# Kernel tuning notes

Hardware: AMD Instinct MI355X
Metric: run time of the kernel (lower is better)

## Reference

```python
import jax, jax.numpy as jnp
import numpy as np

N_U, N_I, E = 100000, 100000, 600000
F_U, F_I, H, OUT = 96, 160, 128, 64
EPS = 1e-5


def _params(key):
    ks = jax.random.split(key, 20)
    n = lambda i, s: (jax.random.normal(ks[i], s, jnp.float32) * 0.05)
    p = {
        # lazy per-type input projections
        'Wp_u': n(0, (F_U, H)), 'bp_u': jnp.zeros((H,), jnp.float32),
        'Wp_i': n(1, (F_I, H)), 'bp_i': jnp.zeros((H,), jnp.float32),
        # layer 0 SAGE (in=H, out=H): lin_l (neighbors, bias), lin_r (root, no bias)
        'Wl0_ui': n(2, (H, H)), 'bl0_ui': jnp.zeros((H,), jnp.float32), 'Wr0_ui': n(3, (H, H)),
        'Wl0_iu': n(4, (H, H)), 'bl0_iu': jnp.zeros((H,), jnp.float32), 'Wr0_iu': n(5, (H, H)),
        'g0_u': jnp.ones((H,), jnp.float32), 'b0_u': jnp.zeros((H,), jnp.float32),
        'g0_i': jnp.ones((H,), jnp.float32), 'b0_i': jnp.zeros((H,), jnp.float32),
        # layer 1 SAGE (in=H, out=OUT)
        'Wl1_ui': n(6, (H, OUT)), 'bl1_ui': jnp.zeros((OUT,), jnp.float32), 'Wr1_ui': n(7, (H, OUT)),
        'Wl1_iu': n(8, (H, OUT)), 'bl1_iu': jnp.zeros((OUT,), jnp.float32), 'Wr1_iu': n(9, (H, OUT)),
        'g1_u': jnp.ones((OUT,), jnp.float32), 'b1_u': jnp.zeros((OUT,), jnp.float32),
        'g1_i': jnp.ones((OUT,), jnp.float32), 'b1_i': jnp.zeros((OUT,), jnp.float32),
    }
    return p


def setup_inputs() -> dict:
    key = jax.random.key(0)
    k0, k1, k2, k3, kp = jax.random.split(key, 5)
    inp = {
        'x_user': jax.random.normal(k0, (N_U, F_U), jnp.float32),
        'x_item': jax.random.normal(k1, (N_I, F_I), jnp.float32),
        'edge_ui': jax.random.randint(k2, (2, E), 0, N_U),  # row0: src user idx, row1: dst item idx
        'edge_iu': jax.random.randint(k3, (2, E), 0, N_I),  # row0: src item idx, row1: dst user idx
    }
    inp.update(_params(kp))
    return inp


def _seg_mean(x_src, src, dst, n_dst):
    # gather source features [E, C], scatter-mean into destinations [n_dst, C]
    msg = x_src[src]
    s = jax.ops.segment_sum(msg, dst, num_segments=n_dst)
    cnt = jax.ops.segment_sum(jnp.ones((dst.shape[0], 1), x_src.dtype), dst, num_segments=n_dst)
    return s / jnp.maximum(cnt, 1.0)


def _sage(x_src, x_dst, edge, Wl, bl, Wr, n_dst):
    agg = _seg_mean(x_src, edge[0], edge[1], n_dst)
    return agg @ Wl + bl + x_dst @ Wr


def _ln(h, g, b):
    m = jnp.mean(h, axis=-1, keepdims=True)
    v = jnp.mean(jnp.square(h - m), axis=-1, keepdims=True)
    return (h - m) * jax.lax.rsqrt(v + EPS) * g + b


def reference(x_user, x_item, edge_ui, edge_iu,
              Wp_u, bp_u, Wp_i, bp_i,
              Wl0_ui, bl0_ui, Wr0_ui, Wl0_iu, bl0_iu, Wr0_iu,
              g0_u, b0_u, g0_i, b0_i,
              Wl1_ui, bl1_ui, Wr1_ui, Wl1_iu, bl1_iu, Wr1_iu,
              g1_u, b1_u, g1_i, b1_i):
    # per-type input projection + ReLU
    h_u = jax.nn.relu(x_user @ Wp_u + bp_u)
    h_i = jax.nn.relu(x_item @ Wp_i + bp_i)
    # layer 0: HeteroConv(sum) of SAGEConv per edge type, then per-type LN + ReLU (dropout = eval identity)
    h_i1 = _sage(h_u, h_i, edge_ui, Wl0_ui, bl0_ui, Wr0_ui, N_I)
    h_u1 = _sage(h_i, h_u, edge_iu, Wl0_iu, bl0_iu, Wr0_iu, N_U)
    h_u1 = jax.nn.relu(_ln(h_u1, g0_u, b0_u))
    h_i1 = jax.nn.relu(_ln(h_i1, g0_i, b0_i))
    # layer 1 (final): SAGE -> LN, no ReLU/dropout
    h_i2 = _sage(h_u1, h_i1, edge_ui, Wl1_ui, bl1_ui, Wr1_ui, N_I)
    h_u2 = _sage(h_i1, h_u1, edge_iu, Wl1_iu, bl1_iu, Wr1_iu, N_U)
    h_u2 = _ln(h_u2, g1_u, b1_u)
    h_i2 = _ln(h_i2, g1_i, b1_i)
    return h_u2, h_i2
```

## Files before the change

### kernel.cpp

```cpp
#include <hip/hip_runtime.h>

typedef __attribute__((ext_vector_type(8))) __bf16 bf16x8;
typedef __attribute__((ext_vector_type(4))) float floatx4;
typedef __attribute__((ext_vector_type(8))) unsigned short ushort8v;
typedef __attribute__((ext_vector_type(4))) unsigned short ushort4v;

namespace {
constexpr int kNU = 100000, kNI = 100000, kE = 600000;
constexpr int kFU = 96, kFI = 160, kH = 128, kOUT = 64;
constexpr float kEPS = 1e-5f;
constexpr int kM = 32;
constexpr int kNCHUNK = 98;
constexpr int kNBLK = kNU / kM;
constexpr int kEB = (kE + 255) / 256;
}

__device__ __forceinline__ unsigned short f2b(float f) {
  unsigned u = __builtin_bit_cast(unsigned, f);
  u += 0x7FFFu + ((u >> 16) & 1u);
  return (unsigned short)(u >> 16);
}
__device__ __forceinline__ float b2f(unsigned short h) {
  return __builtin_bit_cast(float, (unsigned)h << 16);
}
__device__ __forceinline__ void split3(float v, unsigned short& h,
                                       unsigned short& m, unsigned short& l) {
  h = f2b(v);
  const float r1 = v - b2f(h);
  m = f2b(r1);
  const float r2 = r1 - b2f(m);
  l = f2b(r2);
}
__device__ __forceinline__ void split2(float v, unsigned short& h,
                                       unsigned short& m) {
  h = f2b(v);
  m = f2b(v - b2f(h));
}
__device__ __forceinline__ bf16x8 ldb8(const unsigned short* p) {
  return __builtin_bit_cast(bf16x8, *(const ushort8v*)p);
}
__device__ __forceinline__ floatx4 mfma16(bf16x8 a, bf16x8 b, floatx4 c) {
  return __builtin_amdgcn_mfma_f32_16x16x32_bf16(a, b, c, 0, 0, 0);
}
__device__ __forceinline__ unsigned short* ab_ptr(unsigned short* base,
                                                  int plane, int r, int bo) {
  return (unsigned short*)((char*)base + plane * 8192 + r * 256 +
                           (bo ^ ((r & 7) << 4)));
}

struct WcvtArgs {
  const float* src[10];
  unsigned short* dh[10];
  unsigned short* dm[10];
  unsigned short* dl[10];
  int K[10], N[10];
};
__global__ __launch_bounds__(256) void wcvt(WcvtArgs a) {
  const int m = blockIdx.y;
  const int K = a.K[m], N = a.N[m];
  const int idx = blockIdx.x * 256 + threadIdx.x;
  if (idx < K * N) {
    const int n = idx / K, k = idx - n * K;
    unsigned short h, mm, l;
    split3(a.src[m][(size_t)k * N + n], h, mm, l);
    a.dh[m][idx] = h;
    a.dm[m][idx] = mm;
    a.dl[m][idx] = l;
  }
}

__global__ void zero_int(int* __restrict__ p, int n) {
  int i = blockIdx.x * blockDim.x + threadIdx.x;
  const int st = gridDim.x * blockDim.x;
  for (; i < n; i += st) p[i] = 0;
}

__global__ __launch_bounds__(1024) void scanA(const int* __restrict__ cnt_u,
                                              const int* __restrict__ cnt_i,
                                              int* ptr_u, int* ptr_i, int* tot) {
  __shared__ int sh[1024];
  const int dir = blockIdx.y;
  const int* cnt = dir ? cnt_i : cnt_u;
  int* ptr = dir ? ptr_i : ptr_u;
  const int t = threadIdx.x;
  const int i = blockIdx.x * 1024 + t;
  const int v = (i < kNU) ? cnt[i] : 0;
  sh[t] = v;
  __syncthreads();
  for (int o = 1; o < 1024; o <<= 1) {
    const int y = (t >= o) ? sh[t - o] : 0;
    __syncthreads();
    sh[t] += y;
    __syncthreads();
  }
  if (i < kNU) ptr[i] = sh[t] - v;
  if (t == 1023) tot[dir * 128 + blockIdx.x] = sh[1023];
}

__global__ __launch_bounds__(128) void scanB(int* tot) {
  __shared__ int sh[128];
  int* tp = tot + blockIdx.x * 128;
  const int t = threadIdx.x;
  const int v = (t < kNCHUNK) ? tp[t] : 0;
  sh[t] = v;
  __syncthreads();
  for (int o = 1; o < 128; o <<= 1) {
    const int y = (t >= o) ? sh[t - o] : 0;
    __syncthreads();
    sh[t] += y;
    __syncthreads();
  }
  if (t < kNCHUNK) tp[t] = sh[t] - v;
}

__global__ __launch_bounds__(1024) void scanC(int* ptr_u, int* ptr_i,
                                              const int* __restrict__ tot,
                                              int* cur_u, int* cur_i) {
  const int dir = blockIdx.y;
  int* ptr = dir ? ptr_i : ptr_u;
  int* cur = dir ? cur_i : cur_u;
  const int i = blockIdx.x * 1024 + threadIdx.x;
  if (i < kNU) {
    const int v = ptr[i] + tot[dir * 128 + blockIdx.x];
    ptr[i] = v;
    cur[i] = v;
  }
}

template <int F>
__device__ __forceinline__ void proj_body(
    const float* __restrict__ x, const unsigned short* __restrict__ Wh,
    const unsigned short* __restrict__ Wm, const unsigned short* __restrict__ Wl,
    const float* __restrict__ bias, float* __restrict__ out, int blk,
    unsigned short* sh) {
  constexpr int AS = F + 8, KC = F / 32;
  unsigned short* Ah = sh;
  unsigned short* Am = sh + kM * AS;
  unsigned short* Al = sh + 2 * kM * AS;
  const int tid = threadIdx.x;
  const size_t row0 = (size_t)blk * kM;
  for (int c = tid; c < kM * (F / 4); c += 256) {
    const int r = c / (F / 4), j = c % (F / 4);
    const float4 v = *(const float4*)&x[(row0 + r) * F + j * 4];
    const float* vv = &v.x;
    ushort4v h4, m4, l4;
#pragma unroll
    for (int u = 0; u < 4; ++u) {
      unsigned short th, tm, tl;
      split3(vv[u], th, tm, tl);
      h4[u] = th; m4[u] = tm; l4[u] = tl;
    }
    *(ushort4v*)&Ah[r * AS + j * 4] = h4;
    *(ushort4v*)&Am[r * AS + j * 4] = m4;
    *(ushort4v*)&Al[r * AS + j * 4] = l4;
  }
  const int lane = tid & 63, w = tid >> 6, q = lane >> 4, ln = lane & 15;
  floatx4 acc[2][2] = {}, accL[2][2] = {};
  __syncthreads();
#pragma unroll
  for (int kc = 0; kc < KC; ++kc) {
    bf16x8 bh[2], bm[2], bl_[2];
#pragma unroll
    for (int t = 0; t < 2; ++t) {
      const int off = (w * 32 + t * 16 + ln) * F + kc * 32 + q * 8;
      bh[t] = ldb8(&Wh[off]);
      bm[t] = ldb8(&Wm[off]);
      bl_[t] = ldb8(&Wl[off]);
    }
#pragma unroll
    for (int mt = 0; mt < 2; ++mt) {
      const int ro = mt * 16 + ln, co = kc * 32 + q * 8;
      const bf16x8 ah = ldb8(&Ah[ro * AS + co]);
      const bf16x8 am = ldb8(&Am[ro * AS + co]);
      const bf16x8 al = ldb8(&Al[ro * AS + co]);
#pragma unroll
      for (int t = 0; t < 2; ++t) {
        acc[mt][t] = mfma16(ah, bh[t], acc[mt][t]);
        floatx4 cl = accL[mt][t];
        cl = mfma16(ah, bm[t], cl);
        cl = mfma16(am, bh[t], cl);
        cl = mfma16(ah, bl_[t], cl);
        cl = mfma16(al, bh[t], cl);
        cl = mfma16(am, bm[t], cl);
        accL[mt][t] = cl;
      }
    }
  }
#pragma unroll
  for (int t = 0; t < 2; ++t) {
    const int col = w * 32 + t * 16 + ln;
    const float bv = bias[col];
#pragma unroll
    for (int mt = 0; mt < 2; ++mt)
#pragma unroll
      for (int r = 0; r < 4; ++r)
        out[(row0 + mt * 16 + q * 4 + r) * kH + col] =
            fmaxf((acc[mt][t][r] + accL[mt][t][r]) + bv, 0.f);
  }
}

__global__ __launch_bounds__(256) void hist_proj(
    const int* __restrict__ eui, const int* __restrict__ eiu, int* cnt_i,
    int* cnt_u, const float* __restrict__ x,
    const unsigned short* __restrict__ Wh, const unsigned short* __restrict__ Wm,
    const unsigned short* __restrict__ Wl, const float* __restrict__ bias,
    float* __restrict__ out) {
  __shared__ __align__(16) unsigned short sh[3 * kM * (kFU + 8)];
  if (blockIdx.x < kEB) {
    const int e = blockIdx.x * 256 + threadIdx.x;
    if (e < kE) {
      atomicAdd(&cnt_i[eui[kE + e]], 1);
      atomicAdd(&cnt_u[eiu[kE + e]], 1);
    }
  } else {
    proj_body<kFU>(x, Wh, Wm, Wl, bias, out, blockIdx.x - kEB, sh);
  }
}

__global__ __launch_bounds__(256) void fill_proj(
    const int* __restrict__ eui, const int* __restrict__ eiu, int* cur_i,
    int* cur_u, int* __restrict__ col_ui, int* __restrict__ col_iu,
    const float* __restrict__ x, const unsigned short* __restrict__ Wh,
    const unsigned short* __restrict__ Wm, const unsigned short* __restrict__ Wl,
    const float* __restrict__ bias, float* __restrict__ out) {
  __shared__ __align__(16) unsigned short sh[3 * kM * (kFI + 8)];
  if (blockIdx.x < kEB) {
    const int e = blockIdx.x * 256 + threadIdx.x;
    if (e < kE) {
      const int p = atomicAdd(&cur_i[eui[kE + e]], 1);
      col_ui[p] = eui[e];
      const int p2 = atomicAdd(&cur_u[eiu[kE + e]], 1);
      col_iu[p2] = eiu[e];
    }
  } else {
    proj_body<kFI>(x, Wh, Wm, Wl, bias, out, blockIdx.x - kEB, sh);
  }
}

struct AggArgs {
  const float* src[2];
  const int* ptr[2];
  const int* cur[2];
  const int* col[2];
  float* out[2];
};
template <int W>
__global__ __launch_bounds__(256) void agg2(AggArgs a) {
  const int dir = blockIdx.y;
  const int w = threadIdx.x >> 6, lane = threadIdx.x & 63;
  const int row = blockIdx.x * 4 + w;
  const float* __restrict__ feat = a.src[dir];
  const int* __restrict__ col = a.col[dir];
  const int beg = a.ptr[dir][row], end = a.cur[dir][row];
  const float inv = 1.0f / fmaxf((float)(end - beg), 1.0f);
  if (W == 128) {
    float s0 = 0.f, s1 = 0.f;
    int e = beg;
    for (; e + 4 <= end; e += 4) {
      const size_t c0 = col[e], c1 = col[e + 1], c2 = col[e + 2],
                   c3 = col[e + 3];
      const float2 v0 = *(const float2*)&feat[c0 * 128 + lane * 2];
      const float2 v1 = *(const float2*)&feat[c1 * 128 + lane * 2];
      const float2 v2 = *(const float2*)&feat[c2 * 128 + lane * 2];
      const float2 v3 = *(const float2*)&feat[c3 * 128 + lane * 2];
      s0 += v0.x; s1 += v0.y;
      s0 += v1.x; s1 += v1.y;
      s0 += v2.x; s1 += v2.y;
      s0 += v3.x; s1 += v3.y;
    }
    for (; e < end; ++e) {
      const float2 v = *(const float2*)&feat[(size_t)col[e] * 128 + lane * 2];
      s0 += v.x; s1 += v.y;
    }
    float2 o;
    o.x = s0 * inv;
    o.y = s1 * inv;
    *(float2*)&a.out[dir][(size_t)row * 128 + lane * 2] = o;
  } else {
    float s = 0.f;
    int e = beg;
    for (; e + 4 <= end; e += 4) {
      const size_t c0 = col[e], c1 = col[e + 1], c2 = col[e + 2],
                   c3 = col[e + 3];
      const float v0 = feat[c0 * 64 + lane];
      const float v1 = feat[c1 * 64 + lane];
      const float v2 = feat[c2 * 64 + lane];
      const float v3 = feat[c3 * 64 + lane];
      s += v0; s += v1; s += v2; s += v3;
    }
    for (; e < end; ++e) s += feat[(size_t)col[e] * 64 + lane];
    a.out[dir][(size_t)row * 64 + lane] = s * inv;
  }
}

struct FsArgs {
  const float* agg[2];
  const float* root[2];
  const unsigned short *WLh[2], *WLm[2], *WLl[2];
  const unsigned short *WRh[2], *WRm[2], *WRl[2];
  const float *bl[2], *g[2], *b[2];
  float* out[2];
};
__global__ __launch_bounds__(256) void sage0(FsArgs a) {
  constexpr int NOUT = 128;
  __shared__ __align__(16) unsigned short Ab[4 * kM * kH];
  float* Cs = (float*)Ab;
  const int tid = threadIdx.x;
  const int dir = blockIdx.y;
  const size_t row0 = (size_t)blockIdx.x * kM;
  const float* __restrict__ agg = a.agg[dir];
  const float* __restrict__ root = a.root[dir];

  for (int c = tid; c < 2048; c += 256) {
    const int mat = c >> 10, cc = c & 1023, r = cc >> 5, j = cc & 31;
    const float4 v = *(const float4*)((mat ? root : agg) + (row0 + r) * kH + j * 4);
    const float* vv = &v.x;
    ushort4v h4, m4;
#pragma unroll
    for (int u = 0; u < 4; ++u) {
      unsigned short th, tm;
      split2(vv[u], th, tm);
      h4[u] = th; m4[u] = tm;
    }
    *(ushort4v*)ab_ptr(Ab, mat * 2 + 0, r, j * 8) = h4;
    *(ushort4v*)ab_ptr(Ab, mat * 2 + 1, r, j * 8) = m4;
  }

  const int lane = tid & 63, w = tid >> 6, q = lane >> 4, ln = lane & 15;
  floatx4 acc[2][2] = {}, accL[2][2] = {};
  const unsigned short* __restrict__ WLh = a.WLh[dir];
  const unsigned short* __restrict__ WLm = a.WLm[dir];
  const unsigned short* __restrict__ WLl = a.WLl[dir];
  const unsigned short* __restrict__ WRh = a.WRh[dir];
  const unsigned short* __restrict__ WRm = a.WRm[dir];
  const unsigned short* __restrict__ WRl = a.WRl[dir];
  __syncthreads();
#pragma unroll
  for (int kc = 0; kc < 4; ++kc) {
    bf16x8 BL[3][2], BR[3][2];
#pragma unroll
    for (int t = 0; t < 2; ++t) {
      const int off = (w * 32 + t * 16 + ln) * kH + kc * 32 + q * 8;
      BL[0][t] = ldb8(&WLh[off]);
      BL[1][t] = ldb8(&WLm[off]);
      BL[2][t] = ldb8(&WLl[off]);
      BR[0][t] = ldb8(&WRh[off]);
      BR[1][t] = ldb8(&WRm[off]);
      BR[2][t] = ldb8(&WRl[off]);
    }
#pragma unroll
    for (int mt = 0; mt < 2; ++mt) {
      const int ro = mt * 16 + ln, cob = kc * 64 + q * 16;
      const bf16x8 a1h = ldb8(ab_ptr(Ab, 0, ro, cob));
      const bf16x8 a1m = ldb8(ab_ptr(Ab, 1, ro, cob));
      const bf16x8 a2h = ldb8(ab_ptr(Ab, 2, ro, cob));
      const bf16x8 a2m = ldb8(ab_ptr(Ab, 3, ro, cob));
#pragma unroll
      for (int t = 0; t < 2; ++t) {
        floatx4 c = acc[mt][t];
        c = mfma16(a1h, BL[0][t], c);
        c = mfma16(a2h, BR[0][t], c);
        acc[mt][t] = c;
        floatx4 cl = accL[mt][t];
        cl = mfma16(a1h, BL[1][t], cl);
        cl = mfma16(a1m, BL[0][t], cl);
        cl = mfma16(a1h, BL[2][t], cl);
        cl = mfma16(a1m, BL[1][t], cl);
        cl = mfma16(a2h, BR[1][t], cl);
        cl = mfma16(a2m, BR[0][t], cl);
        cl = mfma16(a2h, BR[2][t], cl);
        cl = mfma16(a2m, BR[1][t], cl);
        accL[mt][t] = cl;
      }
    }
  }
  __syncthreads();
  const float* __restrict__ blv = a.bl[dir];
#pragma unroll
  for (int t = 0; t < 2; ++t) {
    const int colx = (w * 2 + t) * 16 + ln;
    const float bv = blv[colx];
#pragma unroll
    for (int mt = 0; mt < 2; ++mt)
#pragma unroll
      for (int r = 0; r < 4; ++r)
        Cs[(mt * 16 + q * 4 + r) * (NOUT + 1) + colx] =
            (acc[mt][t][r] + accL[mt][t][r]) + bv;
  }
  __syncthreads();
  const int r = tid >> 3, sub = tid & 7;
  const float* __restrict__ gg = a.g[dir];
  const float* __restrict__ bb = a.b[dir];
  float vals[16], s = 0.f;
#pragma unroll
  for (int j = 0; j < 16; ++j) {
    const float v = Cs[r * (NOUT + 1) + sub * 16 + j];
    vals[j] = v;
    s += v;
  }
#pragma unroll
  for (int o = 1; o < 8; o <<= 1) s += __shfl_xor(s, o, 64);
  const float mean = s * (1.0f / NOUT);
  float s2 = 0.f;
#pragma unroll
  for (int j = 0; j < 16; ++j) {
    const float d = vals[j] - mean;
    s2 += d * d;
  }
#pragma unroll
  for (int o = 1; o < 8; o <<= 1) s2 += __shfl_xor(s2, o, 64);
  const float rstd = rsqrtf(s2 * (1.0f / NOUT) + kEPS);
  float* op = a.out[dir] + (row0 + r) * NOUT + sub * 16;
#pragma unroll
  for (int j = 0; j < 16; j += 4) {
    float4 o4;
    float* oo = &o4.x;
#pragma unroll
    for (int jj = 0; jj < 4; ++jj)
      oo[jj] = fmaxf((vals[j + jj] - mean) * rstd * gg[sub * 16 + j + jj] +
                         bb[sub * 16 + j + jj],
                     0.f);
    *(float4*)&op[j] = o4;
  }
}

struct ZArgs {
  const float* src[2];
  const unsigned short *Bh[2], *Bm[2], *Bl[2];
  float* out[2];
};
__global__ __launch_bounds__(256) void zproj(ZArgs a) {
  __shared__ __align__(16) unsigned short Ab[2 * kM * kH];
  const int tid = threadIdx.x, dir = blockIdx.y;
  const size_t row0 = (size_t)blockIdx.x * kM;
  const float* __restrict__ src = a.src[dir];
  for (int c = tid; c < 1024; c += 256) {
    const int r = c >> 5, j = c & 31;
    const float4 v = *(const float4*)&src[(row0 + r) * kH + j * 4];
    const float* vv = &v.x;
    ushort4v h4, m4;
#pragma unroll
    for (int u = 0; u < 4; ++u) {
      unsigned short th, tm;
      split2(vv[u], th, tm);
      h4[u] = th; m4[u] = tm;
    }
    *(ushort4v*)ab_ptr(Ab, 0, r, j * 8) = h4;
    *(ushort4v*)ab_ptr(Ab, 1, r, j * 8) = m4;
  }
  const int lane = tid & 63, w = tid >> 6, q = lane >> 4, ln = lane & 15;
  const unsigned short* __restrict__ Bh = a.Bh[dir];
  const unsigned short* __restrict__ Bm = a.Bm[dir];
  const unsigned short* __restrict__ Bl = a.Bl[dir];
  floatx4 acc[2] = {}, accL[2] = {};
  __syncthreads();
#pragma unroll
  for (int kc = 0; kc < 4; ++kc) {
    const int off = (w * 16 + ln) * kH + kc * 32 + q * 8;
    const bf16x8 bh = ldb8(&Bh[off]);
    const bf16x8 bm = ldb8(&Bm[off]);
    const bf16x8 bl_ = ldb8(&Bl[off]);
#pragma unroll
    for (int mt = 0; mt < 2; ++mt) {
      const int ro = mt * 16 + ln, cob = kc * 64 + q * 16;
      const bf16x8 ah = ldb8(ab_ptr(Ab, 0, ro, cob));
      const bf16x8 am = ldb8(ab_ptr(Ab, 1, ro, cob));
      acc[mt] = mfma16(ah, bh, acc[mt]);
      floatx4 cl = accL[mt];
      cl = mfma16(ah, bm, cl);
      cl = mfma16(am, bh, cl);
      cl = mfma16(ah, bl_, cl);
      cl = mfma16(am, bm, cl);
      accL[mt] = cl;
    }
  }
  float* __restrict__ out = a.out[dir];
  const int col = w * 16 + ln;
#pragma unroll
  for (int mt = 0; mt < 2; ++mt)
#pragma unroll
    for (int r = 0; r < 4; ++r)
      out[(row0 + mt * 16 + q * 4 + r) * kOUT + col] =
          acc[mt][r] + accL[mt][r];
}

struct S1Args {
  const float* root[2];
  const float* aggz[2];
  const unsigned short *Bh[2], *Bm[2], *Bl[2];
  const float *bl[2], *g[2], *b[2];
  float* out[2];
};
__global__ __launch_bounds__(256) void sage1(S1Args a) {
  constexpr int NOUT = kOUT;
  __shared__ __align__(16) unsigned short Ab[2 * kM * kH];
  float* Cs = (float*)Ab;
  const int tid = threadIdx.x, dir = blockIdx.y;
  const size_t row0 = (size_t)blockIdx.x * kM;
  const float* __restrict__ root = a.root[dir];
  for (int c = tid; c < 1024; c += 256) {
    const int r = c >> 5, j = c & 31;
    const float4 v = *(const float4*)&root[(row0 + r) * kH + j * 4];
    const float* vv = &v.x;
    ushort4v h4, m4;
#pragma unroll
    for (int u = 0; u < 4; ++u) {
      unsigned short th, tm;
      split2(vv[u], th, tm);
      h4[u] = th; m4[u] = tm;
    }
    *(ushort4v*)ab_ptr(Ab, 0, r, j * 8) = h4;
    *(ushort4v*)ab_ptr(Ab, 1, r, j * 8) = m4;
  }
  const int lane = tid & 63, w = tid >> 6, q = lane >> 4, ln = lane & 15;
  const unsigned short* __restrict__ Bh = a.Bh[dir];
  const unsigned short* __restrict__ Bm = a.Bm[dir];
  const unsigned short* __restrict__ Bl = a.Bl[dir];
  floatx4 acc[2] = {}, accL[2] = {};
  __syncthreads();
#pragma unroll
  for (int kc = 0; kc < 4; ++kc) {
    const int off = (w * 16 + ln) * kH + kc * 32 + q * 8;
    const bf16x8 bh = ldb8(&Bh[off]);
    const bf16x8 bm = ldb8(&Bm[off]);
    const bf16x8 bl_ = ldb8(&Bl[off]);
#pragma unroll
    for (int mt = 0; mt < 2; ++mt) {
      const int ro = mt * 16 + ln, cob = kc * 64 + q * 16;
      const bf16x8 ah = ldb8(ab_ptr(Ab, 0, ro, cob));
      const bf16x8 am = ldb8(ab_ptr(Ab, 1, ro, cob));
      acc[mt] = mfma16(ah, bh, acc[mt]);
      floatx4 cl = accL[mt];
      cl = mfma16(ah, bm, cl);
      cl = mfma16(am, bh, cl);
      cl = mfma16(ah, bl_, cl);
      cl = mfma16(am, bm, cl);
      accL[mt] = cl;
    }
  }
  __syncthreads();
  const float* __restrict__ blv = a.bl[dir];
  {
    const int col = w * 16 + ln;
    const float bv = blv[col];
#pragma unroll
    for (int mt = 0; mt < 2; ++mt)
#pragma unroll
      for (int r = 0; r < 4; ++r)
        Cs[(mt * 16 + q * 4 + r) * (NOUT + 1) + col] =
            (acc[mt][r] + accL[mt][r]) + bv;
  }
  __syncthreads();
  const int r = tid >> 3, sub = tid & 7;
  const float* __restrict__ az = a.aggz[dir];
  const float* __restrict__ gg = a.g[dir];
  const float* __restrict__ bb = a.b[dir];
  float vals[8], s = 0.f;
#pragma unroll
  for (int j = 0; j < 8; ++j) {
    const float v = Cs[r * (NOUT + 1) + sub * 8 + j] +
                    az[(row0 + r) * NOUT + sub * 8 + j];
    vals[j] = v;
    s += v;
  }
#pragma unroll
  for (int o = 1; o < 8; o <<= 1) s += __shfl_xor(s, o, 64);
  const float mean = s * (1.0f / NOUT);
  float s2 = 0.f;
#pragma unroll
  for (int j = 0; j < 8; ++j) {
    const float d = vals[j] - mean;
    s2 += d * d;
  }
#pragma unroll
  for (int o = 1; o < 8; o <<= 1) s2 += __shfl_xor(s2, o, 64);
  const float rstd = rsqrtf(s2 * (1.0f / NOUT) + kEPS);
  float* op = a.out[dir] + (row0 + r) * NOUT + sub * 8;
#pragma unroll
  for (int j = 0; j < 8; j += 4) {
    float4 o4;
    float* oo = &o4.x;
#pragma unroll
    for (int jj = 0; jj < 4; ++jj)
      oo[jj] = (vals[j + jj] - mean) * rstd * gg[sub * 8 + j + jj] +
               bb[sub * 8 + j + jj];
    *(float4*)&op[j] = o4;
  }
}

extern "C" void kernel_launch(void* const* d_in, const int* in_sizes, int n_in,
                              void* d_out, int out_size, void* d_ws, size_t ws_size,
                              hipStream_t stream) {
  (void)in_sizes; (void)n_in; (void)out_size; (void)ws_size;
  const float* x_u    = (const float*)d_in[0];
  const float* x_i    = (const float*)d_in[1];
  const int*   e_ui   = (const int*)d_in[2];
  const int*   e_iu   = (const int*)d_in[3];
  const float* Wp_u   = (const float*)d_in[4];
  const float* bp_u   = (const float*)d_in[5];
  const float* Wp_i   = (const float*)d_in[6];
  const float* bp_i   = (const float*)d_in[7];
  const float* Wl0_ui = (const float*)d_in[8];
  const float* bl0_ui = (const float*)d_in[9];
  const float* Wr0_ui = (const float*)d_in[10];
  const float* Wl0_iu = (const float*)d_in[11];
  const float* bl0_iu = (const float*)d_in[12];
  const float* Wr0_iu = (const float*)d_in[13];
  const float* g0_u   = (const float*)d_in[14];
  const float* b0_u   = (const float*)d_in[15];
  const float* g0_i   = (const float*)d_in[16];
  const float* b0_i   = (const float*)d_in[17];
  const float* Wl1_ui = (const float*)d_in[18];
  const float* bl1_ui = (const float*)d_in[19];
  const float* Wr1_ui = (const float*)d_in[20];
  const float* Wl1_iu = (const float*)d_in[21];
  const float* bl1_iu = (const float*)d_in[22];
  const float* Wr1_iu = (const float*)d_in[23];
  const float* g1_u   = (const float*)d_in[24];
  const float* b1_u   = (const float*)d_in[25];
  const float* g1_i   = (const float*)d_in[26];
  const float* b1_i   = (const float*)d_in[27];

  float* pf = (float*)d_ws;
  const size_t NH = (size_t)kNU * kH;
  float* hu0 = pf;
  float* hi0 = pf + NH;
  float* b2  = pf + 2 * NH;
  float* b3  = pf + 3 * NH;
  float* Zu = hu0;
  float* Zi = hu0 + (size_t)kNU * kOUT;
  float* aggzI = hi0;
  float* aggzU = hi0 + (size_t)kNU * kOUT;
  unsigned short* wh = (unsigned short*)(pf + 4 * NH);
  unsigned short* wm = wh + 131072;
  unsigned short* wl = wm + 131072;
  int* pi = (int*)(wl + 131072);
  int* cnt_u = pi; pi += kNU;
  int* cnt_i = pi; pi += kNU;
  int* ptr_u = pi; pi += kNU;
  int* ptr_i = pi; pi += kNU;
  int* cur_u = pi; pi += kNU;
  int* cur_i = pi; pi += kNU;
  int* tot   = pi; pi += 2 * 128;
  int* col_ui = pi; pi += kE;
  int* col_iu = pi; pi += kE;

  const int oPu = 0, oPi = 12288, o0Lui = 32768, o0Rui = 49152,
            o0Liu = 65536, o0Riu = 81920, o1Lui = 98304, o1Rui = 106496,
            o1Liu = 114688, o1Riu = 122880;

  float* out_u = (float*)d_out;
  float* out_i = out_u + (size_t)kNU * kOUT;

  WcvtArgs wa;
  const float* wsrc[10] = {Wp_u, Wp_i, Wl0_ui, Wr0_ui, Wl0_iu, Wr0_iu,
                           Wl1_ui, Wr1_ui, Wl1_iu, Wr1_iu};
  const int woff[10] = {oPu, oPi, o0Lui, o0Rui, o0Liu, o0Riu,
                        o1Lui, o1Rui, o1Liu, o1Riu};
  const int wK[10] = {kFU, kFI, kH, kH, kH, kH, kH, kH, kH, kH};
  const int wN[10] = {kH, kH, kH, kH, kH, kH, kOUT, kOUT, kOUT, kOUT};
  for (int i = 0; i < 10; ++i) {
    wa.src[i] = wsrc[i];
    wa.dh[i] = wh + woff[i];
    wa.dm[i] = wm + woff[i];
    wa.dl[i] = wl + woff[i];
    wa.K[i] = wK[i];
    wa.N[i] = wN[i];
  }
  wcvt<<<dim3(80, 10), 256, 0, stream>>>(wa);

  zero_int<<<256, 256, 0, stream>>>(cnt_u, 2 * kNU);
  hist_proj<<<kEB + kNBLK, 256, 0, stream>>>(e_ui, e_iu, cnt_i, cnt_u, x_u,
                                             wh + oPu, wm + oPu, wl + oPu,
                                             bp_u, hu0);
  scanA<<<dim3(kNCHUNK, 2), 1024, 0, stream>>>(cnt_u, cnt_i, ptr_u, ptr_i, tot);
  scanB<<<2, 128, 0, stream>>>(tot);
  scanC<<<dim3(kNCHUNK, 2), 1024, 0, stream>>>(ptr_u, ptr_i, tot, cur_u, cur_i);
  fill_proj<<<kEB + kNBLK, 256, 0, stream>>>(e_ui, e_iu, cur_i, cur_u, col_ui,
                                             col_iu, x_i, wh + oPi, wm + oPi,
                                             wl + oPi, bp_i, hi0);

  AggArgs g0;
  g0.src[0] = hu0; g0.ptr[0] = ptr_i; g0.cur[0] = cur_i; g0.col[0] = col_ui;
  g0.out[0] = b2;
  g0.src[1] = hi0; g0.ptr[1] = ptr_u; g0.cur[1] = cur_u; g0.col[1] = col_iu;
  g0.out[1] = b3;
  agg2<kH><<<dim3(kNU / 4, 2), 256, 0, stream>>>(g0);

  FsArgs a0;
  a0.agg[0] = b2; a0.root[0] = hi0;
  a0.WLh[0] = wh + o0Lui; a0.WLm[0] = wm + o0Lui; a0.WLl[0] = wl + o0Lui;
  a0.WRh[0] = wh + o0Rui; a0.WRm[0] = wm + o0Rui; a0.WRl[0] = wl + o0Rui;
  a0.bl[0] = bl0_ui; a0.g[0] = g0_i; a0.b[0] = b0_i; a0.out[0] = b2;
  a0.agg[1] = b3; a0.root[1] = hu0;
  a0.WLh[1] = wh + o0Liu; a0.WLm[1] = wm + o0Liu; a0.WLl[1] = wl + o0Liu;
  a0.WRh[1] = wh + o0Riu; a0.WRm[1] = wm + o0Riu; a0.WRl[1] = wl + o0Riu;
  a0.bl[1] = bl0_iu; a0.g[1] = g0_u; a0.b[1] = b0_u; a0.out[1] = b3;
  sage0<<<dim3(kNBLK, 2), 256, 0, stream>>>(a0);

  ZArgs zp;
  zp.src[0] = b3;
  zp.Bh[0] = wh + o1Lui; zp.Bm[0] = wm + o1Lui; zp.Bl[0] = wl + o1Lui;
  zp.out[0] = Zu;
  zp.src[1] = b2;
  zp.Bh[1] = wh + o1Liu; zp.Bm[1] = wm + o1Liu; zp.Bl[1] = wl + o1Liu;
  zp.out[1] = Zi;
  zproj<<<dim3(kNBLK, 2), 256, 0, stream>>>(zp);

  AggArgs g1;
  g1.src[0] = Zu; g1.ptr[0] = ptr_i; g1.cur[0] = cur_i; g1.col[0] = col_ui;
  g1.out[0] = aggzI;
  g1.src[1] = Zi; g1.ptr[1] = ptr_u; g1.cur[1] = cur_u; g1.col[1] = col_iu;
  g1.out[1] = aggzU;
  agg2<kOUT><<<dim3(kNU / 4, 2), 256, 0, stream>>>(g1);

  S1Args s1;
  s1.root[0] = b2; s1.aggz[0] = aggzI;
  s1.Bh[0] = wh + o1Rui; s1.Bm[0] = wm + o1Rui; s1.Bl[0] = wl + o1Rui;
  s1.bl[0] = bl1_ui; s1.g[0] = g1_i; s1.b[0] = b1_i; s1.out[0] = out_i;
  s1.root[1] = b3; s1.aggz[1] = aggzU;
  s1.Bh[1] = wh + o1Riu; s1.Bm[1] = wm + o1Riu; s1.Bl[1] = wl + o1Riu;
  s1.bl[1] = bl1_iu; s1.g[1] = g1_u; s1.b[1] = b1_u; s1.out[1] = out_u;
  sage1<<<dim3(kNBLK, 2), 256, 0, stream>>>(s1);
}
```

Baseline: 816.3 us.

## Partition CSR build atomics, widen gather unroll, drop low split-bf16 terms

The histogram and fill phases now launch eight times as many edge blocks. Each block only handles destinations in its own eighth of the node range, so atomics stay local and column writes cluster. The neighbour gather loops take eight edges per step with predicated loads, which raises memory-level parallelism. The layer GEMMs drop the third (low) bf16 split and the second-order correction products, so they do fewer MFMAs and weight loads at some loss of precision. Launch bounds now request higher occupancy, and the sage1 epilogue reads aggregates with vector loads.

Measured after the change: 774.7 us. -5.1%, faster.

```diff
diff --git a/kernel.cpp b/kernel.cpp
--- a/kernel.cpp
+++ b/kernel.cpp
@@ -13,6 +13,7 @@
 constexpr int kNCHUNK = 98;
 constexpr int kNBLK = kNU / kM;
 constexpr int kEB = (kE + 255) / 256;
+constexpr int kPART = kNU / 8;
 }
 
 __device__ __forceinline__ unsigned short f2b(float f) {
@@ -199,41 +200,51 @@
   }
 }
 
-__global__ __launch_bounds__(256) void hist_proj(
+__global__ __launch_bounds__(256, 4) void hist_proj(
     const int* __restrict__ eui, const int* __restrict__ eiu, int* cnt_i,
     int* cnt_u, const float* __restrict__ x,
     const unsigned short* __restrict__ Wh, const unsigned short* __restrict__ Wm,
     const unsigned short* __restrict__ Wl, const float* __restrict__ bias,
     float* __restrict__ out) {
   __shared__ __align__(16) unsigned short sh[3 * kM * (kFU + 8)];
-  if (blockIdx.x < kEB) {
-    const int e = blockIdx.x * 256 + threadIdx.x;
+  if (blockIdx.x < 8 * kEB) {
+    const int part = blockIdx.x & 7, slice = blockIdx.x >> 3;
+    const int e = slice * 256 + threadIdx.x;
     if (e < kE) {
-      atomicAdd(&cnt_i[eui[kE + e]], 1);
-      atomicAdd(&cnt_u[eiu[kE + e]], 1);
+      const int di = eui[kE + e];
+      if (di / kPART == part) atomicAdd(&cnt_i[di], 1);
+      const int du = eiu[kE + e];
+      if (du / kPART == part) atomicAdd(&cnt_u[du], 1);
     }
   } else {
-    proj_body<kFU>(x, Wh, Wm, Wl, bias, out, blockIdx.x - kEB, sh);
-  }
-}
-
-__global__ __launch_bounds__(256) void fill_proj(
+    proj_body<kFU>(x, Wh, Wm, Wl, bias, out, blockIdx.x - 8 * kEB, sh);
+  }
+}
+
+__global__ __launch_bounds__(256, 4) void fill_proj(
     const int* __restrict__ eui, const int* __restrict__ eiu, int* cur_i,
     int* cur_u, int* __restrict__ col_ui, int* __restrict__ col_iu,
     const float* __restrict__ x, const unsigned short* __restrict__ Wh,
     const unsigned short* __restrict__ Wm, const unsigned short* __restrict__ Wl,
     const float* __restrict__ bias, float* __restrict__ out) {
   __shared__ __align__(16) unsigned short sh[3 * kM * (kFI + 8)];
-  if (blockIdx.x < kEB) {
-    const int e = blockIdx.x * 256 + threadIdx.x;
+  if (blockIdx.x < 8 * kEB) {
+    const int part = blockIdx.x & 7, slice = blockIdx.x >> 3;
+    const int e = slice * 256 + threadIdx.x;
     if (e < kE) {
-      const int p = atomicAdd(&cur_i[eui[kE + e]], 1);
-      col_ui[p] = eui[e];
-      const int p2 = atomicAdd(&cur_u[eiu[kE + e]], 1);
-      col_iu[p2] = eiu[e];
+      const int di = eui[kE + e];
+      if (di / kPART == part) {
+        const int p = atomicAdd(&cur_i[di], 1);
+        col_ui[p] = eui[e];
+      }
+      const int du = eiu[kE + e];
+      if (du / kPART == part) {
+        const int p2 = atomicAdd(&cur_u[du], 1);
+        col_iu[p2] = eiu[e];
+      }
     }
   } else {
-    proj_body<kFI>(x, Wh, Wm, Wl, bias, out, blockIdx.x - kEB, sh);
+    proj_body<kFI>(x, Wh, Wm, Wl, bias, out, blockIdx.x - 8 * kEB, sh);
   }
 }
 
@@ -255,22 +266,15 @@
   const float inv = 1.0f / fmaxf((float)(end - beg), 1.0f);
   if (W == 128) {
     float s0 = 0.f, s1 = 0.f;
-    int e = beg;
-    for (; e + 4 <= end; e += 4) {
-      const size_t c0 = col[e], c1 = col[e + 1], c2 = col[e + 2],
-                   c3 = col[e + 3];
-      const float2 v0 = *(const float2*)&feat[c0 * 128 + lane * 2];
-      const float2 v1 = *(const float2*)&feat[c1 * 128 + lane * 2];
-      const float2 v2 = *(const float2*)&feat[c2 * 128 + lane * 2];
-      const float2 v3 = *(const float2*)&feat[c3 * 128 + lane * 2];
-      s0 += v0.x; s1 += v0.y;
-      s0 += v1.x; s1 += v1.y;
-      s0 += v2.x; s1 += v2.y;
-      s0 += v3.x; s1 += v3.y;
-    }
-    for (; e < end; ++e) {
-      const float2 v = *(const float2*)&feat[(size_t)col[e] * 128 + lane * 2];
-      s0 += v.x; s1 += v.y;
+    for (int e = beg; e < end; e += 8) {
+      const int n = end - e;
+      float2 v[8];
+#pragma unroll
+      for (int j = 0; j < 8; ++j)
+        if (j < n) v[j] = *(const float2*)&feat[(size_t)col[e + j] * 128 + lane * 2];
+#pragma unroll
+      for (int j = 0; j < 8; ++j)
+        if (j < n) { s0 += v[j].x; s1 += v[j].y; }
     }
     float2 o;
     o.x = s0 * inv;
@@ -278,17 +282,16 @@
     *(float2*)&a.out[dir][(size_t)row * 128 + lane * 2] = o;
   } else {
     float s = 0.f;
-    int e = beg;
-    for (; e + 4 <= end; e += 4) {
-      const size_t c0 = col[e], c1 = col[e + 1], c2 = col[e + 2],
-                   c3 = col[e + 3];
-      const float v0 = feat[c0 * 64 + lane];
-      const float v1 = feat[c1 * 64 + lane];
-      const float v2 = feat[c2 * 64 + lane];
-      const float v3 = feat[c3 * 64 + lane];
-      s += v0; s += v1; s += v2; s += v3;
-    }
-    for (; e < end; ++e) s += feat[(size_t)col[e] * 64 + lane];
+    for (int e = beg; e < end; e += 8) {
+      const int n = end - e;
+      float v[8];
+#pragma unroll
+      for (int j = 0; j < 8; ++j)
+        if (j < n) v[j] = feat[(size_t)col[e + j] * 64 + lane];
+#pragma unroll
+      for (int j = 0; j < 8; ++j)
+        if (j < n) s += v[j];
+    }
     a.out[dir][(size_t)row * 64 + lane] = s * inv;
   }
 }
@@ -296,12 +299,12 @@
 struct FsArgs {
   const float* agg[2];
   const float* root[2];
-  const unsigned short *WLh[2], *WLm[2], *WLl[2];
-  const unsigned short *WRh[2], *WRm[2], *WRl[2];
+  const unsigned short *WLh[2], *WLm[2];
+  const unsigned short *WRh[2], *WRm[2];
   const float *bl[2], *g[2], *b[2];
   float* out[2];
 };
-__global__ __launch_bounds__(256) void sage0(FsArgs a) {
+__global__ __launch_bounds__(256, 4) void sage0(FsArgs a) {
   constexpr int NOUT = 128;
   __shared__ __align__(16) unsigned short Ab[4 * kM * kH];
   float* Cs = (float*)Ab;
@@ -330,23 +333,19 @@
   floatx4 acc[2][2] = {}, accL[2][2] = {};
   const unsigned short* __restrict__ WLh = a.WLh[dir];
   const unsigned short* __restrict__ WLm = a.WLm[dir];
-  const unsigned short* __restrict__ WLl = a.WLl[dir];
   const unsigned short* __restrict__ WRh = a.WRh[dir];
   const unsigned short* __restrict__ WRm = a.WRm[dir];
-  const unsigned short* __restrict__ WRl = a.WRl[dir];
   __syncthreads();
 #pragma unroll
   for (int kc = 0; kc < 4; ++kc) {
-    bf16x8 BL[3][2], BR[3][2];
+    bf16x8 BL[2][2], BR[2][2];
 #pragma unroll
     for (int t = 0; t < 2; ++t) {
       const int off = (w * 32 + t * 16 + ln) * kH + kc * 32 + q * 8;
       BL[0][t] = ldb8(&WLh[off]);
       BL[1][t] = ldb8(&WLm[off]);
-      BL[2][t] = ldb8(&WLl[off]);
       BR[0][t] = ldb8(&WRh[off]);
       BR[1][t] = ldb8(&WRm[off]);
-      BR[2][t] = ldb8(&WRl[off]);
     }
 #pragma unroll
     for (int mt = 0; mt < 2; ++mt) {
@@ -364,12 +363,8 @@
         floatx4 cl = accL[mt][t];
         cl = mfma16(a1h, BL[1][t], cl);
         cl = mfma16(a1m, BL[0][t], cl);
-        cl = mfma16(a1h, BL[2][t], cl);
-        cl = mfma16(a1m, BL[1][t], cl);
         cl = mfma16(a2h, BR[1][t], cl);
         cl = mfma16(a2m, BR[0][t], cl);
-        cl = mfma16(a2h, BR[2][t], cl);
-        cl = mfma16(a2m, BR[1][t], cl);
         accL[mt][t] = cl;
       }
     }
@@ -426,10 +421,10 @@
 
 struct ZArgs {
   const float* src[2];
-  const unsigned short *Bh[2], *Bm[2], *Bl[2];
+  const unsigned short *Bh[2], *Bm[2];
   float* out[2];
 };
-__global__ __launch_bounds__(256) void zproj(ZArgs a) {
+__global__ __launch_bounds__(256, 4) void zproj(ZArgs a) {
   __shared__ __align__(16) unsigned short Ab[2 * kM * kH];
   const int tid = threadIdx.x, dir = blockIdx.y;
   const size_t row0 = (size_t)blockIdx.x * kM;
@@ -451,7 +446,6 @@
   const int lane = tid & 63, w = tid >> 6, q = lane >> 4, ln = lane & 15;
   const unsigned short* __restrict__ Bh = a.Bh[dir];
   const unsigned short* __restrict__ Bm = a.Bm[dir];
-  const unsigned short* __restrict__ Bl = a.Bl[dir];
   floatx4 acc[2] = {}, accL[2] = {};
   __syncthreads();
 #pragma unroll
@@ -459,7 +453,6 @@
     const int off = (w * 16 + ln) * kH + kc * 32 + q * 8;
     const bf16x8 bh = ldb8(&Bh[off]);
     const bf16x8 bm = ldb8(&Bm[off]);
-    const bf16x8 bl_ = ldb8(&Bl[off]);
 #pragma unroll
     for (int mt = 0; mt < 2; ++mt) {
       const int ro = mt * 16 + ln, cob = kc * 64 + q * 16;
@@ -469,8 +462,6 @@
       floatx4 cl = accL[mt];
       cl = mfma16(ah, bm, cl);
       cl = mfma16(am, bh, cl);
-      cl = mfma16(ah, bl_, cl);
-      cl = mfma16(am, bm, cl);
       accL[mt] = cl;
     }
   }
@@ -487,11 +478,11 @@
 struct S1Args {
   const float* root[2];
   const float* aggz[2];
-  const unsigned short *Bh[2], *Bm[2], *Bl[2];
+  const unsigned short *Bh[2], *Bm[2];
   const float *bl[2], *g[2], *b[2];
   float* out[2];
 };
-__global__ __launch_bounds__(256) void sage1(S1Args a) {
+__global__ __launch_bounds__(256, 4) void sage1(S1Args a) {
   constexpr int NOUT = kOUT;
   __shared__ __align__(16) unsigned short Ab[2 * kM * kH];
   float* Cs = (float*)Ab;
@@ -515,7 +506,6 @@
   const int lane = tid & 63, w = tid >> 6, q = lane >> 4, ln = lane & 15;
   const unsigned short* __restrict__ Bh = a.Bh[dir];
   const unsigned short* __restrict__ Bm = a.Bm[dir];
-  const unsigned short* __restrict__ Bl = a.Bl[dir];
   floatx4 acc[2] = {}, accL[2] = {};
   __syncthreads();
 #pragma unroll
@@ -523,7 +513,6 @@
     const int off = (w * 16 + ln) * kH + kc * 32 + q * 8;
     const bf16x8 bh = ldb8(&Bh[off]);
     const bf16x8 bm = ldb8(&Bm[off]);
-    const bf16x8 bl_ = ldb8(&Bl[off]);
 #pragma unroll
     for (int mt = 0; mt < 2; ++mt) {
       const int ro = mt * 16 + ln, cob = kc * 64 + q * 16;
@@ -533,8 +522,6 @@
       floatx4 cl = accL[mt];
       cl = mfma16(ah, bm, cl);
       cl = mfma16(am, bh, cl);
-      cl = mfma16(ah, bl_, cl);
-      cl = mfma16(am, bm, cl);
       accL[mt] = cl;
     }
   }
@@ -555,14 +542,18 @@
   const float* __restrict__ az = a.aggz[dir];
   const float* __restrict__ gg = a.g[dir];
   const float* __restrict__ bb = a.b[dir];
+  const float4 az0 = *(const float4*)&az[(row0 + r) * NOUT + sub * 8];
+  const float4 az1 = *(const float4*)&az[(row0 + r) * NOUT + sub * 8 + 4];
+  const float* azv = &az0.x;
   float vals[8], s = 0.f;
 #pragma unroll
   for (int j = 0; j < 8; ++j) {
     const float v = Cs[r * (NOUT + 1) + sub * 8 + j] +
-                    az[(row0 + r) * NOUT + sub * 8 + j];
+                    (j < 4 ? (&az0.x)[j] : (&az1.x)[j - 4]);
     vals[j] = v;
     s += v;
   }
+  (void)azv;
 #pragma unroll
   for (int o = 1; o < 8; o <<= 1) s += __shfl_xor(s, o, 64);
   const float mean = s * (1.0f / NOUT);
@@ -670,15 +661,15 @@
   wcvt<<<dim3(80, 10), 256, 0, stream>>>(wa);
 
   zero_int<<<256, 256, 0, stream>>>(cnt_u, 2 * kNU);
-  hist_proj<<<kEB + kNBLK, 256, 0, stream>>>(e_ui, e_iu, cnt_i, cnt_u, x_u,
-                                             wh + oPu, wm + oPu, wl + oPu,
-                                             bp_u, hu0);
+  hist_proj<<<8 * kEB + kNBLK, 256, 0, stream>>>(e_ui, e_iu, cnt_i, cnt_u, x_u,
+                                                 wh + oPu, wm + oPu, wl + oPu,
+                                                 bp_u, hu0);
   scanA<<<dim3(kNCHUNK, 2), 1024, 0, stream>>>(cnt_u, cnt_i, ptr_u, ptr_i, tot);
   scanB<<<2, 128, 0, stream>>>(tot);
   scanC<<<dim3(kNCHUNK, 2), 1024, 0, stream>>>(ptr_u, ptr_i, tot, cur_u, cur_i);
-  fill_proj<<<kEB + kNBLK, 256, 0, stream>>>(e_ui, e_iu, cur_i, cur_u, col_ui,
-                                             col_iu, x_i, wh + oPi, wm + oPi,
-                                             wl + oPi, bp_i, hi0);
+  fill_proj<<<8 * kEB + kNBLK, 256, 0, stream>>>(e_ui, e_iu, cur_i, cur_u,
+                                                 col_ui, col_iu, x_i, wh + oPi,
+                                                 wm + oPi, wl + oPi, bp_i, hi0);
 
   AggArgs g0;
   g0.src[0] = hu0; g0.ptr[0] = ptr_i; g0.cur[0] = cur_i; g0.col[0] = col_ui;
@@ -689,21 +680,21 @@
 
   FsArgs a0;
   a0.agg[0] = b2; a0.root[0] = hi0;
-  a0.WLh[0] = wh + o0Lui; a0.WLm[0] = wm + o0Lui; a0.WLl[0] = wl + o0Lui;
-  a0.WRh[0] = wh + o0Rui; a0.WRm[0] = wm + o0Rui; a0.WRl[0] = wl + o0Rui;
+  a0.WLh[0] = wh + o0Lui; a0.WLm[0] = wm + o0Lui;
+  a0.WRh[0] = wh + o0Rui; a0.WRm[0] = wm + o0Rui;
   a0.bl[0] = bl0_ui; a0.g[0] = g0_i; a0.b[0] = b0_i; a0.out[0] = b2;
   a0.agg[1] = b3; a0.root[1] = hu0;
-  a0.WLh[1] = wh + o0Liu; a0.WLm[1] = wm + o0Liu; a0.WLl[1] = wl + o0Liu;
-  a0.WRh[1] = wh + o0Riu; a0.WRm[1] = wm + o0Riu; a0.WRl[1] = wl + o0Riu;
+  a0.WLh[1] = wh + o0Liu; a0.WLm[1] = wm + o0Liu;
+  a0.WRh[1] = wh + o0Riu; a0.WRm[1] = wm + o0Riu;
   a0.bl[1] = bl0_iu; a0.g[1] = g0_u; a0.b[1] = b0_u; a0.out[1] = b3;
   sage0<<<dim3(kNBLK, 2), 256, 0, stream>>>(a0);
 
   ZArgs zp;
   zp.src[0] = b3;
-  zp.Bh[0] = wh + o1Lui; zp.Bm[0] = wm + o1Lui; zp.Bl[0] = wl + o1Lui;
+  zp.Bh[0] = wh + o1Lui; zp.Bm[0] = wm + o1Lui;
   zp.out[0] = Zu;
   zp.src[1] = b2;
-  zp.Bh[1] = wh + o1Liu; zp.Bm[1] = wm + o1Liu; zp.Bl[1] = wl + o1Liu;
+  zp.Bh[1] = wh + o1Liu; zp.Bm[1] = wm + o1Liu;
   zp.out[1] = Zi;
   zproj<<<dim3(kNBLK, 2), 256, 0, stream>>>(zp);
 
@@ -716,10 +707,10 @@
 
   S1Args s1;
   s1.root[0] = b2; s1.aggz[0] = aggzI;
-  s1.Bh[0] = wh + o1Rui; s1.Bm[0] = wm + o1Rui; s1.Bl[0] = wl + o1Rui;
+  s1.Bh[0] = wh + o1Rui; s1.Bm[0] = wm + o1Rui;
   s1.bl[0] = bl1_ui; s1.g[0] = g1_i; s1.b[0] = b1_i; s1.out[0] = out_i;
   s1.root[1] = b3; s1.aggz[1] = aggzU;
-  s1.Bh[1] = wh + o1Riu; s1.Bm[1] = wm + o1Riu; s1.Bl[1] = wl + o1Riu;
+  s1.Bh[1] = wh + o1Riu; s1.Bm[1] = wm + o1Riu;
   s1.bl[1] = bl1_iu; s1.g[1] = g1_u; s1.b[1] = b1_u; s1.out[1] = out_u;
   sage1<<<dim3(kNBLK, 2), 256, 0, stream>>>(s1);
 }
```
